# Kernel tuning notes

Measured on AMD Instinct MI355X. Metric: run time of the kernel, lower is better.

## Reference

```python
import jax, jax.numpy as jnp
import numpy as np

N = 100000   # nodes
E = 1000000  # edges (before self-loops)
G = 64       # graphs in batch
IN, HID, OUT = 128, 64, 1


def setup_inputs() -> dict:
    key = jax.random.key(0)
    ks = jax.random.split(key, 24)
    inp = {
        "x": jax.random.normal(ks[0], (N, IN), jnp.float32),
        "adj": jax.random.randint(ks[1], (2, E), 0, N, jnp.int32),
        "batch": jnp.sort(jax.random.randint(ks[2], (N,), 0, G, jnp.int32)),
    }
    i = 3
    dims = [(IN, HID), (HID, HID), (HID, HID)]
    for l, (di, do) in enumerate(dims, start=1):
        inp[f"W{l}"] = jax.random.normal(ks[i], (di, do), jnp.float32) * (1.0 / np.sqrt(di)); i += 1
        inp[f"a_src{l}"] = jax.random.normal(ks[i], (do,), jnp.float32) * 0.1; i += 1
        inp[f"a_dst{l}"] = jax.random.normal(ks[i], (do,), jnp.float32) * 0.1; i += 1
        inp[f"b{l}"] = jnp.zeros((do,), jnp.float32); i += 1
    inp["linnews_W"] = jax.random.normal(ks[i], (IN, HID), jnp.float32) * (1.0 / np.sqrt(IN)); i += 1
    inp["linnews_b"] = jnp.zeros((HID,), jnp.float32)
    inp["lin0_W"] = jax.random.normal(ks[i], (HID, HID), jnp.float32) * (1.0 / np.sqrt(HID)); i += 1
    inp["lin0_b"] = jnp.zeros((HID,), jnp.float32)
    inp["lin1_W"] = jax.random.normal(ks[i], (2 * HID, OUT), jnp.float32) * (1.0 / np.sqrt(2 * HID)); i += 1
    inp["lin1_b"] = jnp.zeros((OUT,), jnp.float32)
    return inp


def _gat_layer(x, src, dst, W, a_src, a_dst, b):
    # PyG GATConv, heads=1, self-loops already appended to (src, dst).
    h = x @ W                                        # [N, HID]
    e = (h @ a_src)[src] + (h @ a_dst)[dst]          # [E'] edge scores
    e = jax.nn.leaky_relu(e, 0.2)
    # segment softmax over incoming edges of each dst node
    m = jax.ops.segment_max(e, dst, num_segments=N)
    num = jnp.exp(e - m[dst])
    den = jax.ops.segment_sum(num, dst, num_segments=N)
    coef = num / (den[dst] + 1e-16)                  # [E']
    out = jax.ops.segment_sum(coef[:, None] * h[src], dst, num_segments=N)
    return out + b


def reference(x, adj, batch, W1, a_src1, a_dst1, b1, W2, a_src2, a_dst2, b2,
              W3, a_src3, a_dst3, b3, linnews_W, linnews_b, lin0_W, lin0_b,
              lin1_W, lin1_b):
    loop = jnp.arange(N, dtype=adj.dtype)
    src = jnp.concatenate([adj[0], loop])
    dst = jnp.concatenate([adj[1], loop])

    h = jax.nn.relu(_gat_layer(x, src, dst, W1, a_src1, a_dst1, b1))
    h = jax.nn.relu(_gat_layer(h, src, dst, W2, a_src2, a_dst2, b2))
    h = jax.nn.relu(_gat_layer(h, src, dst, W3, a_src3, a_dst3, b3))

    # global max pool per graph
    h = jax.ops.segment_max(h, batch, num_segments=G)        # [G, HID]
    h = jax.nn.relu(h @ lin0_W + lin0_b)

    # root node of each graph = first index with that batch id
    root = jax.ops.segment_min(jnp.arange(N), batch, num_segments=G)  # [G]
    news = jax.nn.relu(x[root] @ linnews_W + linnews_b)      # [G, HID]

    out = jnp.concatenate([h, news], axis=-1) @ lin1_W + lin1_b
    return jax.nn.sigmoid(out)                               # [G, 1]
```

## Files before the change

kernel.cpp:

```cpp
#include <hip/hip_runtime.h>
#include <hip/hip_fp16.h>
#include <cstdint>
#include <type_traits>

#define THREADS 256
#define NBLK 64
#define BPAD 512
#define LINBLK 640
#define ECAP 1024

typedef _Float16 half8 __attribute__((ext_vector_type(8)));
typedef float v4f __attribute__((ext_vector_type(4)));
typedef float v2f __attribute__((ext_vector_type(2)));

__global__ __launch_bounds__(256) void hist_kernel(const int* __restrict__ dst_e,
                                                   int* __restrict__ hist, int E, int chunk,
                                                   float* __restrict__ pool, int* __restrict__ root,
                                                   int G) {
  __shared__ int hcnt[BPAD];
  int t = threadIdx.x, blk = blockIdx.x;
  if (blk == 0) {
    for (int i = t; i < G * 64; i += 256) pool[i] = 0.0f;
    for (int i = t; i < G; i += 256) root[i] = 0x7fffffff;
  }
  for (int i = t; i < BPAD; i += 256) hcnt[i] = 0;
  __syncthreads();
  int s = blk * chunk, e = s + chunk;
  if (e > E) e = E;
  for (int i = s + t; i < e; i += 256) atomicAdd(&hcnt[dst_e[i] >> 8], 1);
  __syncthreads();
  for (int b = t; b < BPAD; b += 256) hist[b * NBLK + blk] = hcnt[b];
}

__global__ __launch_bounds__(256) void hscan_kernel(int* __restrict__ hist) {
  __shared__ int part[256];
  const int PER = (BPAD * NBLK) / 256;
  int t = threadIdx.x;
  int base = t * PER;
  int sum = 0;
  for (int k = 0; k < PER; k++) sum += hist[base + k];
  part[t] = sum;
  __syncthreads();
  int own = sum;
  for (int off = 1; off < 256; off <<= 1) {
    int v = (t >= off) ? part[t - off] : 0;
    __syncthreads();
    part[t] += v;
    __syncthreads();
  }
  int run = part[t] - own;
  for (int k = 0; k < PER; k++) {
    int h = hist[base + k];
    hist[base + k] = run;
    run += h;
  }
}

__global__ __launch_bounds__(256) void scatter_kernel(const int* __restrict__ src_e,
                                                      const int* __restrict__ dst_e,
                                                      const int* __restrict__ hist,
                                                      unsigned int* __restrict__ ebuf,
                                                      int E, int chunk) {
  __shared__ int cur[BPAD];
  int t = threadIdx.x, blk = blockIdx.x;
  for (int b = t; b < BPAD; b += 256) cur[b] = hist[b * NBLK + blk];
  __syncthreads();
  int s = blk * chunk, e = s + chunk;
  if (e > E) e = E;
  for (int i = s + t; i < e; i += 256) {
    int d = dst_e[i];
    unsigned int sv = (unsigned int)src_e[i];
    int slot = atomicAdd(&cur[d >> 8], 1);
    ebuf[slot] = (sv << 8) | (unsigned int)(d & 255);
  }
}

__global__ __launch_bounds__(256) void build_kernel(const unsigned int* __restrict__ ebuf,
                                                    const int* __restrict__ hist,
                                                    int* __restrict__ row_start,
                                                    int* __restrict__ csr_src,
                                                    int N, int E) {
  __shared__ int counts[256];
  __shared__ int sc[256];
  __shared__ int curw[256];
  int t = threadIdx.x, b = blockIdx.x;
  int nbase = b * 256;
  int ebase = hist[b * NBLK];
  int eend = hist[(b + 1) * NBLK];
  counts[t] = 0;
  __syncthreads();
  int ecount = eend - ebase;
  for (int i = t; i < ecount; i += 256)
    atomicAdd(&counts[ebuf[ebase + i] & 255u], 1);
  __syncthreads();
  int n = nbase + t;
  int val = (n < N) ? counts[t] + 1 : 0;
  sc[t] = val;
  __syncthreads();
  int own = val;
  for (int off = 1; off < 256; off <<= 1) {
    int v = (t >= off) ? sc[t - off] : 0;
    __syncthreads();
    sc[t] += v;
    __syncthreads();
  }
  int myloc = sc[t] - own;
  int rowb = ebase + nbase;
  if (n < N) {
    row_start[n] = rowb + myloc;
    csr_src[rowb + myloc + counts[t]] = n;
    if (n == N - 1) row_start[N] = rowb + myloc + counts[t] + 1;
  }
  curw[t] = rowb + myloc;
  __syncthreads();
  for (int i = t; i < ecount; i += 256) {
    unsigned int ev = ebuf[ebase + i];
    int pos = atomicAdd(&curw[ev & 255u], 1);
    csr_src[pos] = (int)(ev >> 8);
  }
}

__device__ __forceinline__ void store_row_fp8(const _Float16* hp, unsigned char* dst) {
  unsigned int d[4];
#pragma unroll
  for (int q = 0; q < 4; q++) {
    float f0 = (float)hp[q * 4 + 0], f1 = (float)hp[q * 4 + 1];
    float f2 = (float)hp[q * 4 + 2], f3 = (float)hp[q * 4 + 3];
    unsigned int w0 = __builtin_amdgcn_cvt_pk_fp8_f32(f0, f1, 0, false);
    d[q] = __builtin_amdgcn_cvt_pk_fp8_f32(f2, f3, w0, true);
  }
  uint4 v; v.x = d[0]; v.y = d[1]; v.z = d[2]; v.w = d[3];
  *(uint4*)dst = v;
}

template <int K, typename TIN>
__global__ __launch_bounds__(256) void lin_attn_kernel(
    const TIN* __restrict__ in, const float* __restrict__ W,
    const float* __restrict__ a_src, const float* __restrict__ a_dst,
    unsigned char* __restrict__ h8, float* __restrict__ as_, float* __restrict__ ad_,
    int N, int nwaves) {
  constexpr int NKC = K / 32;
  __shared__ _Float16 sh[4][16 * 72];
  const int t = threadIdx.x;
  const int lane = t & 63, w = t >> 6;
  const int col = lane & 15, quad = lane >> 4;
  const int wid = blockIdx.x * 4 + w;

  half8 bf[4][NKC];
#pragma unroll
  for (int nt = 0; nt < 4; nt++)
#pragma unroll
    for (int kc = 0; kc < NKC; kc++) {
      half8 v;
#pragma unroll
      for (int j = 0; j < 8; j++)
        v[j] = (_Float16)W[(kc * 32 + quad * 8 + j) * 64 + nt * 16 + col];
      bf[nt][kc] = v;
    }
  float sa[4], sd[4];
#pragma unroll
  for (int nt = 0; nt < 4; nt++) {
    sa[nt] = a_src[nt * 16 + col];
    sd[nt] = a_dst[nt * 16 + col];
  }

  const int ntiles = (N + 15) >> 4;
  for (int tile = wid; tile < ntiles; tile += nwaves) {
    const int nb = tile << 4;
    int nodeA = nb + col;
    if (nodeA >= N) nodeA = N - 1;
    const TIN* arow = in + (size_t)nodeA * K + quad * 8;

    v4f acc[4];
#pragma unroll
    for (int nt = 0; nt < 4; nt++) acc[nt] = (v4f){0.f, 0.f, 0.f, 0.f};

#pragma unroll
    for (int kc = 0; kc < NKC; kc++) {
      half8 a;
      if constexpr (std::is_same<TIN, float>::value) {
        float4 f0 = *(const float4*)(arow + kc * 32);
        float4 f1 = *(const float4*)(arow + kc * 32 + 4);
        a[0] = (_Float16)f0.x; a[1] = (_Float16)f0.y;
        a[2] = (_Float16)f0.z; a[3] = (_Float16)f0.w;
        a[4] = (_Float16)f1.x; a[5] = (_Float16)f1.y;
        a[6] = (_Float16)f1.z; a[7] = (_Float16)f1.w;
      } else {
        a = *(const half8*)(arow + kc * 32);
      }
#pragma unroll
      for (int nt = 0; nt < 4; nt++)
        acc[nt] = __builtin_amdgcn_mfma_f32_16x16x32_f16(a, bf[nt][kc], acc[nt], 0, 0, 0);
    }

    float ps[4], pd[4];
#pragma unroll
    for (int r = 0; r < 4; r++) { ps[r] = 0.f; pd[r] = 0.f; }
#pragma unroll
    for (int nt = 0; nt < 4; nt++)
#pragma unroll
      for (int r = 0; r < 4; r++) {
        ps[r] += acc[nt][r] * sa[nt];
        pd[r] += acc[nt][r] * sd[nt];
      }
#pragma unroll
    for (int r = 0; r < 4; r++)
#pragma unroll
      for (int m = 1; m < 16; m <<= 1) {
        ps[r] += __shfl_xor(ps[r], m);
        pd[r] += __shfl_xor(pd[r], m);
      }
    if (col == 0) {
#pragma unroll
      for (int r = 0; r < 4; r++) {
        int node = nb + quad * 4 + r;
        if (node < N) { as_[node] = ps[r]; ad_[node] = pd[r]; }
      }
    }

#pragma unroll
    for (int nt = 0; nt < 4; nt++)
#pragma unroll
      for (int r = 0; r < 4; r++)
        sh[w][(quad * 4 + r) * 72 + nt * 16 + col] = (_Float16)acc[nt][r];
    int nr = lane >> 2, c4 = lane & 3;
    int node = nb + nr;
    if (node < N)
      store_row_fp8(&sh[w][nr * 72 + c4 * 16], h8 + (size_t)node * 64 + c4 * 16);
  }
}

__device__ __forceinline__ void agg_block_stage(
    const uint2* __restrict__ h8v, const float* __restrict__ as_in,
    const int* __restrict__ csr_src, int* __restrict__ s_src,
    float* __restrict__ s_as, int t, int co,
    int e0, int eEnd, int rs, int re, float adn,
    float4& A0, float4& A1, float& den) {
  bool first = true;
  for (int cs = e0; cs < eEnd; cs += ECAP) {
    int ce = cs + ECAP; if (ce > eEnd) ce = eEnd;
    int cnt = ce - cs;
    if (!first) __syncthreads();
    first = false;
    for (int i = t; i < cnt; i += 512) {
      int s0 = csr_src[cs + i];
      bool has2 = (i + 256 < cnt);
      int s1 = has2 ? csr_src[cs + i + 256] : s0;
      float av0 = as_in[s0];
      float av1 = as_in[s1];
      s_src[i] = s0; s_as[i] = av0;
      if (has2) { s_src[i + 256] = s1; s_as[i + 256] = av1; }
    }
    __syncthreads();
    int a0 = rs > cs ? rs : cs;
    int a1 = re < ce ? re : ce;
    if (a0 >= a1) continue;

    auto loadhv = [&](int sb, uint2* hv) {
#pragma unroll
      for (int j = 0; j < 4; j++) {
        int sj = sb + j;
        int ii = ((sj < a1) ? sj : (a1 - 1)) - cs;
        hv[j] = h8v[(size_t)s_src[ii] * 8 + co];
      }
    };
    auto consume = [&](int sb, const uint2* hv) {
#pragma unroll
      for (int j = 0; j < 4; j++) {
        int sj = sb + j;
        int ii = ((sj < a1) ? sj : (a1 - 1)) - cs;
        float e = s_as[ii] + adn;
        e = fmaxf(e, 0.2f * e);
        float c = (sj < a1) ? __expf(e) : 0.f;
        v2f f0 = __builtin_amdgcn_cvt_pk_f32_fp8(hv[j].x, false);
        v2f f1 = __builtin_amdgcn_cvt_pk_f32_fp8(hv[j].x, true);
        v2f f2 = __builtin_amdgcn_cvt_pk_f32_fp8(hv[j].y, false);
        v2f f3 = __builtin_amdgcn_cvt_pk_f32_fp8(hv[j].y, true);
        den += c;
        A0.x += c * f0[0]; A0.y += c * f0[1]; A0.z += c * f1[0]; A0.w += c * f1[1];
        A1.x += c * f2[0]; A1.y += c * f2[1]; A1.z += c * f3[0]; A1.w += c * f3[1];
      }
    };

    uint2 hvA[4];
    int s = a0;
    loadhv(s, hvA);
    for (s = a0 + 4; s < a1; s += 4) {
      uint2 hvB[4];
      loadhv(s, hvB);
      consume(s - 4, hvA);
#pragma unroll
      for (int j = 0; j < 4; j++) hvA[j] = hvB[j];
    }
    consume(s - 4, hvA);
  }
}

__device__ __forceinline__ void agg_finish(const float4& A0, const float4& A1,
                                           float den, const float* __restrict__ bprev,
                                           int co, _Float16* o) {
  float inv = 1.0f / (den + 1e-16f);
  float4 b0 = *(const float4*)&bprev[co * 8];
  float4 b1 = *(const float4*)&bprev[co * 8 + 4];
  o[0] = (_Float16)fmaxf(A0.x * inv + b0.x, 0.f);
  o[1] = (_Float16)fmaxf(A0.y * inv + b0.y, 0.f);
  o[2] = (_Float16)fmaxf(A0.z * inv + b0.z, 0.f);
  o[3] = (_Float16)fmaxf(A0.w * inv + b0.w, 0.f);
  o[4] = (_Float16)fmaxf(A1.x * inv + b1.x, 0.f);
  o[5] = (_Float16)fmaxf(A1.y * inv + b1.y, 0.f);
  o[6] = (_Float16)fmaxf(A1.z * inv + b1.z, 0.f);
  o[7] = (_Float16)fmaxf(A1.w * inv + b1.w, 0.f);
}

__global__ __launch_bounds__(256) void agg_lin_kernel(
    const uint2* __restrict__ h8in, const float* __restrict__ as_in,
    const float* __restrict__ ad_in, const int* __restrict__ csr_src,
    const int* __restrict__ row_start, const float* __restrict__ bprev,
    const float* __restrict__ W, const float* __restrict__ a_src,
    const float* __restrict__ a_dst, unsigned char* __restrict__ h8out,
    float* __restrict__ as_out, float* __restrict__ ad_out, int N) {
  __shared__ int s_src[ECAP];
  __shared__ float s_as[ECAP];
  __shared__ _Float16 shh[32][72];
  __shared__ _Float16 sht[2][16 * 72];
  const int t = threadIdx.x;
  const int lane = t & 63, w = t >> 6;
  const int base = blockIdx.x * 32;

  {
    const int ng = lane >> 3, co = lane & 7;
    const int ln = w * 8 + ng;
    int n = base + ln;
    int nc = (n < N) ? n : (N - 1);
    int rs = row_start[nc], re = row_start[nc + 1];
    float adn = ad_in[nc];
    int nend = base + 32; if (nend > N) nend = N;
    int e0 = row_start[base], eEnd = row_start[nend];
    float4 A0 = make_float4(0.f, 0.f, 0.f, 0.f);
    float4 A1 = make_float4(0.f, 0.f, 0.f, 0.f);
    float den = 0.f;
    agg_block_stage(h8in, as_in, csr_src, s_src, s_as, t, co,
                    e0, eEnd, rs, re, adn, A0, A1, den);
    _Float16 o[8];
    agg_finish(A0, A1, den, bprev, co, o);
    *(float4*)&shh[ln][co * 8] = *(float4*)o;
  }
  __syncthreads();
  if (w >= 2) return;

  const int col = lane & 15, quad = lane >> 4;
  half8 bf[4][2];
  float sa[4], sd[4];
#pragma unroll
  for (int nt = 0; nt < 4; nt++) {
#pragma unroll
    for (int kc = 0; kc < 2; kc++) {
      half8 v;
#pragma unroll
      for (int j = 0; j < 8; j++)
        v[j] = (_Float16)W[(kc * 32 + quad * 8 + j) * 64 + nt * 16 + col];
      bf[nt][kc] = v;
    }
    sa[nt] = a_src[nt * 16 + col];
    sd[nt] = a_dst[nt * 16 + col];
  }

  const int nb = base + w * 16;
  v4f acc[4];
#pragma unroll
  for (int nt = 0; nt < 4; nt++) acc[nt] = (v4f){0.f, 0.f, 0.f, 0.f};
#pragma unroll
  for (int kc = 0; kc < 2; kc++) {
    half8 a = *(const half8*)&shh[w * 16 + col][kc * 32 + quad * 8];
#pragma unroll
    for (int nt = 0; nt < 4; nt++)
      acc[nt] = __builtin_amdgcn_mfma_f32_16x16x32_f16(a, bf[nt][kc], acc[nt], 0, 0, 0);
  }

  float ps[4], pd[4];
#pragma unroll
  for (int r = 0; r < 4; r++) { ps[r] = 0.f; pd[r] = 0.f; }
#pragma unroll
  for (int nt = 0; nt < 4; nt++)
#pragma unroll
    for (int r = 0; r < 4; r++) {
      ps[r] += acc[nt][r] * sa[nt];
      pd[r] += acc[nt][r] * sd[nt];
    }
#pragma unroll
  for (int r = 0; r < 4; r++)
#pragma unroll
    for (int m = 1; m < 16; m <<= 1) {
      ps[r] += __shfl_xor(ps[r], m);
      pd[r] += __shfl_xor(pd[r], m);
    }
  if (col == 0) {
#pragma unroll
    for (int r = 0; r < 4; r++) {
      int node = nb + quad * 4 + r;
      if (node < N) { as_out[node] = ps[r]; ad_out[node] = pd[r]; }
    }
  }

#pragma unroll
  for (int nt = 0; nt < 4; nt++)
#pragma unroll
    for (int r = 0; r < 4; r++)
      sht[w][(quad * 4 + r) * 72 + nt * 16 + col] = (_Float16)acc[nt][r];
  int nr = lane >> 2, c4 = lane & 3;
  int node = nb + nr;
  if (node < N)
    store_row_fp8(&sht[w][nr * 72 + c4 * 16], h8out + (size_t)node * 64 + c4 * 16);
}

__global__ __launch_bounds__(256) void agg_pool_kernel(
    const uint2* __restrict__ h8in, const float* __restrict__ as_in,
    const float* __restrict__ ad_in, const int* __restrict__ csr_src,
    const int* __restrict__ row_start, const float* __restrict__ bprev,
    const int* __restrict__ batch, float* __restrict__ pool,
    int* __restrict__ root, int N) {
  __shared__ int s_src[ECAP];
  __shared__ float s_as[ECAP];
  __shared__ float red[4][64];
  const int t = threadIdx.x;
  const int lane = t & 63, w = t >> 6;
  const int ng = lane >> 3, co = lane & 7;
  const int ln = w * 8 + ng;
  const int base = blockIdx.x * 32;
  int n = base + ln;
  int nc = (n < N) ? n : (N - 1);
  int rs = row_start[nc], re = row_start[nc + 1];
  float adn = ad_in[nc];
  int nend = base + 32; if (nend > N) nend = N;
  int e0 = row_start[base], eEnd = row_start[nend];
  float4 A0 = make_float4(0.f, 0.f, 0.f, 0.f);
  float4 A1 = make_float4(0.f, 0.f, 0.f, 0.f);
  float den = 0.f;
  agg_block_stage(h8in, as_in, csr_src, s_src, s_as, t, co,
                  e0, eEnd, rs, re, adn, A0, A1, den);
  _Float16 o[8];
  agg_finish(A0, A1, den, bprev, co, o);
  float ov[8];
#pragma unroll
  for (int j = 0; j < 8; j++) ov[j] = (float)o[j];

  int g = batch[nc];
  if (co == 0 && n < N) {
    if (n == 0 || batch[n - 1] != g) atomicMin(&root[g], n);
  }

  int bstart = base;
  int bend = base + 31; if (bend >= N) bend = N - 1;
  int gfirst = batch[bstart];
  int glast = batch[bend];
  if (gfirst == glast) {
#pragma unroll
    for (int m = 8; m < 64; m <<= 1)
#pragma unroll
      for (int j = 0; j < 8; j++) ov[j] = fmaxf(ov[j], __shfl_xor(ov[j], m));
    if (ng == 0)
#pragma unroll
      for (int j = 0; j < 8; j++) red[w][co * 8 + j] = ov[j];
    __syncthreads();
    if (t < 64) {
      float m0 = fmaxf(red[0][t], red[1][t]);
      float m1 = fmaxf(red[2][t], red[3][t]);
      atomicMax((int*)&pool[(size_t)gfirst * 64 + t], __float_as_int(fmaxf(m0, m1)));
    }
  } else {
#pragma unroll
    for (int j = 0; j < 8; j++)
      if (n < N) atomicMax((int*)&pool[(size_t)g * 64 + co * 8 + j], __float_as_int(ov[j]));
  }
}

__global__ void final_kernel(const float* __restrict__ pool, const int* __restrict__ root,
                             const float* __restrict__ x,
                             const float* __restrict__ lin0_W, const float* __restrict__ lin0_b,
                             const float* __restrict__ linnews_W, const float* __restrict__ linnews_b,
                             const float* __restrict__ lin1_W, const float* __restrict__ lin1_b,
                             float* __restrict__ out, int G, int N) {
  int t = threadIdx.x;
  int lane = t & 63, w = t >> 6;
  int g = blockIdx.x * 4 + w;
  if (g >= G) return;
  float hp = 0.f;
  for (int k = 0; k < 64; k++) hp += pool[(size_t)g * 64 + k] * lin0_W[k * 64 + lane];
  hp = fmaxf(hp + lin0_b[lane], 0.f);
  int r = root[g]; if (r > N - 1) r = N - 1; if (r < 0) r = 0;
  float nw = 0.f;
  for (int k = 0; k < 128; k++) nw += x[(size_t)r * 128 + k] * linnews_W[k * 64 + lane];
  nw = fmaxf(nw + linnews_b[lane], 0.f);
  float p = hp * lin1_W[lane] + nw * lin1_W[64 + lane];
  for (int k = 1; k < 64; k <<= 1) p += __shfl_xor(p, k);
  if (lane == 0) out[g] = 1.0f / (1.0f + __expf(-(p + lin1_b[0])));
}

extern "C" void kernel_launch(void* const* d_in, const int* in_sizes, int n_in,
                              void* d_out, int out_size, void* d_ws, size_t ws_size,
                              hipStream_t stream) {
  (void)n_in; (void)ws_size;
  const float* x      = (const float*)d_in[0];
  const int*   adj    = (const int*)d_in[1];
  const int*   batch  = (const int*)d_in[2];
  const float* W1     = (const float*)d_in[3];
  const float* asrc1  = (const float*)d_in[4];
  const float* adst1  = (const float*)d_in[5];
  const float* b1     = (const float*)d_in[6];
  const float* W2     = (const float*)d_in[7];
  const float* asrc2  = (const float*)d_in[8];
  const float* adst2  = (const float*)d_in[9];
  const float* b2     = (const float*)d_in[10];
  const float* W3     = (const float*)d_in[11];
  const float* asrc3  = (const float*)d_in[12];
  const float* adst3  = (const float*)d_in[13];
  const float* b3     = (const float*)d_in[14];
  const float* lnW    = (const float*)d_in[15];
  const float* lnb    = (const float*)d_in[16];
  const float* l0W    = (const float*)d_in[17];
  const float* l0b    = (const float*)d_in[18];
  const float* l1W    = (const float*)d_in[19];
  const float* l1b    = (const float*)d_in[20];
  float* outp = (float*)d_out;

  const int N = in_sizes[2];
  const int E = in_sizes[1] / 2;
  const int Etot = E + N;
  const int G = out_size;
  const int B = (N + 255) / 256;

  const int* src_e = adj;
  const int* dst_e = adj + E;

  uintptr_t p = (uintptr_t)d_ws;
  auto alloc = [&](size_t bytes) -> void* {
    void* r = (void*)p;
    p += (bytes + 255) & ~(size_t)255;
    return r;
  };
  int*      hist      = (int*)alloc((size_t)BPAD * NBLK * 4);
  int*      row_start = (int*)alloc((size_t)(N + 1) * 4);
  int*      csr_src   = (int*)alloc((size_t)Etot * 4);
  unsigned int* ebuf  = (unsigned int*)alloc((size_t)E * 4);
  unsigned char* hA   = (unsigned char*)alloc((size_t)N * 64);
  unsigned char* hB   = (unsigned char*)alloc((size_t)N * 64);
  float*    asA       = (float*)alloc((size_t)N * 4);
  float*    adA       = (float*)alloc((size_t)N * 4);
  float*    asB       = (float*)alloc((size_t)N * 4);
  float*    adB       = (float*)alloc((size_t)N * 4);
  float*    pool      = (float*)alloc((size_t)G * 64 * 4);
  int*      root      = (int*)alloc((size_t)G * 4);

  int chunk = (E + NBLK - 1) / NBLK;
  hist_kernel<<<dim3(NBLK), dim3(256), 0, stream>>>(dst_e, hist, E, chunk, pool, root, G);
  hscan_kernel<<<dim3(1), dim3(256), 0, stream>>>(hist);
  scatter_kernel<<<dim3(NBLK), dim3(256), 0, stream>>>(src_e, dst_e, hist, ebuf, E, chunk);
  build_kernel<<<dim3(B), dim3(256), 0, stream>>>(ebuf, hist, row_start, csr_src, N, E);

  const int aggGrid = (N + 31) / 32;
  const int nwaves = LINBLK * 4;

  lin_attn_kernel<128, float><<<dim3(LINBLK), dim3(256), 0, stream>>>(
      x, W1, asrc1, adst1, hA, asA, adA, N, nwaves);
  agg_lin_kernel<<<dim3(aggGrid), dim3(256), 0, stream>>>(
      (const uint2*)hA, asA, adA, csr_src, row_start, b1, W2, asrc2, adst2, hB, asB, adB, N);
  agg_lin_kernel<<<dim3(aggGrid), dim3(256), 0, stream>>>(
      (const uint2*)hB, asB, adB, csr_src, row_start, b2, W3, asrc3, adst3, hA, asA, adA, N);
  agg_pool_kernel<<<dim3(aggGrid), dim3(256), 0, stream>>>(
      (const uint2*)hA, asA, adA, csr_src, row_start, b3, batch, pool, root, N);

  final_kernel<<<dim3((G + 3) / 4), dim3(256), 0, stream>>>(
      pool, root, x, l0W, l0b, lnW, lnb, l1W, l1b, outp, G, N);
}
```

Measured before the change: 294.7 us.

## Split layer-1 linear projection across CSR-build kernels as extra blocks

Removes the standalone layer-1 linear/attention kernel and splits its node tiles into four quarters. Each quarter runs on extra blocks appended to one of the four CSR-construction kernels (hist, scan, scatter, build). The aim is to fill the mostly idle GPU during those low-occupancy graph-building kernels and drop one launch. The cost is more shared memory and registers in those kernels, and the build work may now compete with the matmul blocks for compute units.

```diff
diff --git a/kernel.cpp b/kernel.cpp
--- a/kernel.cpp
+++ b/kernel.cpp
@@ -6,19 +6,129 @@
 #define THREADS 256
 #define NBLK 64
 #define BPAD 512
-#define LINBLK 640
 #define ECAP 1024
+#define LINB 392
 
 typedef _Float16 half8 __attribute__((ext_vector_type(8)));
 typedef float v4f __attribute__((ext_vector_type(4)));
 typedef float v2f __attribute__((ext_vector_type(2)));
 
-__global__ __launch_bounds__(256) void hist_kernel(const int* __restrict__ dst_e,
-                                                   int* __restrict__ hist, int E, int chunk,
-                                                   float* __restrict__ pool, int* __restrict__ root,
-                                                   int G) {
+__device__ __forceinline__ void store_row_fp8(const _Float16* hp, unsigned char* dst) {
+  unsigned int d[4];
+#pragma unroll
+  for (int q = 0; q < 4; q++) {
+    float f0 = (float)hp[q * 4 + 0], f1 = (float)hp[q * 4 + 1];
+    float f2 = (float)hp[q * 4 + 2], f3 = (float)hp[q * 4 + 3];
+    unsigned int w0 = __builtin_amdgcn_cvt_pk_fp8_f32(f0, f1, 0, false);
+    d[q] = __builtin_amdgcn_cvt_pk_fp8_f32(f2, f3, w0, true);
+  }
+  uint4 v; v.x = d[0]; v.y = d[1]; v.z = d[2]; v.w = d[3];
+  *(uint4*)dst = v;
+}
+
+__device__ __forceinline__ void lin1_run(
+    const float* __restrict__ in, const float* __restrict__ W,
+    const float* __restrict__ a_src, const float* __restrict__ a_dst,
+    unsigned char* __restrict__ h8, float* __restrict__ as_, float* __restrict__ ad_,
+    int N, int tile0, int tile1, int wid, int nwaves, _Float16* shw) {
+  const int lane = threadIdx.x & 63;
+  const int col = lane & 15, quad = lane >> 4;
+
+  half8 bf[4][4];
+#pragma unroll
+  for (int nt = 0; nt < 4; nt++)
+#pragma unroll
+    for (int kc = 0; kc < 4; kc++) {
+      half8 v;
+#pragma unroll
+      for (int j = 0; j < 8; j++)
+        v[j] = (_Float16)W[(kc * 32 + quad * 8 + j) * 64 + nt * 16 + col];
+      bf[nt][kc] = v;
+    }
+  float sa[4], sd[4];
+#pragma unroll
+  for (int nt = 0; nt < 4; nt++) {
+    sa[nt] = a_src[nt * 16 + col];
+    sd[nt] = a_dst[nt * 16 + col];
+  }
+
+  for (int tile = tile0 + wid; tile < tile1; tile += nwaves) {
+    const int nb = tile << 4;
+    int nodeA = nb + col;
+    if (nodeA >= N) nodeA = N - 1;
+    const float* arow = in + (size_t)nodeA * 128 + quad * 8;
+
+    v4f acc[4];
+#pragma unroll
+    for (int nt = 0; nt < 4; nt++) acc[nt] = (v4f){0.f, 0.f, 0.f, 0.f};
+
+#pragma unroll
+    for (int kc = 0; kc < 4; kc++) {
+      float4 f0 = *(const float4*)(arow + kc * 32);
+      float4 f1 = *(const float4*)(arow + kc * 32 + 4);
+      half8 a;
+      a[0] = (_Float16)f0.x; a[1] = (_Float16)f0.y;
+      a[2] = (_Float16)f0.z; a[3] = (_Float16)f0.w;
+      a[4] = (_Float16)f1.x; a[5] = (_Float16)f1.y;
+      a[6] = (_Float16)f1.z; a[7] = (_Float16)f1.w;
+#pragma unroll
+      for (int nt = 0; nt < 4; nt++)
+        acc[nt] = __builtin_amdgcn_mfma_f32_16x16x32_f16(a, bf[nt][kc], acc[nt], 0, 0, 0);
+    }
+
+    float ps[4], pd[4];
+#pragma unroll
+    for (int r = 0; r < 4; r++) { ps[r] = 0.f; pd[r] = 0.f; }
+#pragma unroll
+    for (int nt = 0; nt < 4; nt++)
+#pragma unroll
+      for (int r = 0; r < 4; r++) {
+        ps[r] += acc[nt][r] * sa[nt];
+        pd[r] += acc[nt][r] * sd[nt];
+      }
+#pragma unroll
+    for (int r = 0; r < 4; r++)
+#pragma unroll
+      for (int m = 1; m < 16; m <<= 1) {
+        ps[r] += __shfl_xor(ps[r], m);
+        pd[r] += __shfl_xor(pd[r], m);
+      }
+    if (col == 0) {
+#pragma unroll
+      for (int r = 0; r < 4; r++) {
+        int node = nb + quad * 4 + r;
+        if (node < N) { as_[node] = ps[r]; ad_[node] = pd[r]; }
+      }
+    }
+
+#pragma unroll
+    for (int nt = 0; nt < 4; nt++)
+#pragma unroll
+      for (int r = 0; r < 4; r++)
+        shw[(quad * 4 + r) * 72 + nt * 16 + col] = (_Float16)acc[nt][r];
+    int nr = lane >> 2, c4 = lane & 3;
+    int node = nb + nr;
+    if (node < N)
+      store_row_fp8(&shw[nr * 72 + c4 * 16], h8 + (size_t)node * 64 + c4 * 16);
+  }
+}
+
+#define LIN_ARGS const float* __restrict__ x, const float* __restrict__ W1, \
+                 const float* __restrict__ a1s, const float* __restrict__ a1d, \
+                 unsigned char* __restrict__ h8, float* __restrict__ lin_as, \
+                 float* __restrict__ lin_ad, int Nn, int tile0, int tile1, int nlw
+
+__global__ __launch_bounds__(256) void hist_lin_kernel(
+    const int* __restrict__ dst_e, int* __restrict__ hist, int E, int chunk,
+    float* __restrict__ pool, int* __restrict__ root, int G, LIN_ARGS) {
   __shared__ int hcnt[BPAD];
+  __shared__ _Float16 sh[4][16 * 72];
   int t = threadIdx.x, blk = blockIdx.x;
+  if (blk >= NBLK) {
+    int wid = (blk - NBLK) * 4 + (t >> 6);
+    lin1_run(x, W1, a1s, a1d, h8, lin_as, lin_ad, Nn, tile0, tile1, wid, nlw, sh[t >> 6]);
+    return;
+  }
   if (blk == 0) {
     for (int i = t; i < G * 64; i += 256) pool[i] = 0.0f;
     for (int i = t; i < G; i += 256) root[i] = 0x7fffffff;
@@ -32,10 +142,16 @@
   for (int b = t; b < BPAD; b += 256) hist[b * NBLK + blk] = hcnt[b];
 }
 
-__global__ __launch_bounds__(256) void hscan_kernel(int* __restrict__ hist) {
+__global__ __launch_bounds__(256) void hscan_lin_kernel(int* __restrict__ hist, LIN_ARGS) {
   __shared__ int part[256];
+  __shared__ _Float16 sh[4][16 * 72];
+  int t = threadIdx.x, blk = blockIdx.x;
+  if (blk >= 1) {
+    int wid = (blk - 1) * 4 + (t >> 6);
+    lin1_run(x, W1, a1s, a1d, h8, lin_as, lin_ad, Nn, tile0, tile1, wid, nlw, sh[t >> 6]);
+    return;
+  }
   const int PER = (BPAD * NBLK) / 256;
-  int t = threadIdx.x;
   int base = t * PER;
   int sum = 0;
   for (int k = 0; k < PER; k++) sum += hist[base + k];
@@ -56,13 +172,18 @@
   }
 }
 
-__global__ __launch_bounds__(256) void scatter_kernel(const int* __restrict__ src_e,
-                                                      const int* __restrict__ dst_e,
-                                                      const int* __restrict__ hist,
-                                                      unsigned int* __restrict__ ebuf,
-                                                      int E, int chunk) {
+__global__ __launch_bounds__(256) void scatter_lin_kernel(
+    const int* __restrict__ src_e, const int* __restrict__ dst_e,
+    const int* __restrict__ hist, unsigned int* __restrict__ ebuf,
+    int E, int chunk, LIN_ARGS) {
   __shared__ int cur[BPAD];
+  __shared__ _Float16 sh[4][16 * 72];
   int t = threadIdx.x, blk = blockIdx.x;
+  if (blk >= NBLK) {
+    int wid = (blk - NBLK) * 4 + (t >> 6);
+    lin1_run(x, W1, a1s, a1d, h8, lin_as, lin_ad, Nn, tile0, tile1, wid, nlw, sh[t >> 6]);
+    return;
+  }
   for (int b = t; b < BPAD; b += 256) cur[b] = hist[b * NBLK + blk];
   __syncthreads();
   int s = blk * chunk, e = s + chunk;
@@ -75,15 +196,20 @@
   }
 }
 
-__global__ __launch_bounds__(256) void build_kernel(const unsigned int* __restrict__ ebuf,
-                                                    const int* __restrict__ hist,
-                                                    int* __restrict__ row_start,
-                                                    int* __restrict__ csr_src,
-                                                    int N, int E) {
+__global__ __launch_bounds__(256) void build_lin_kernel(
+    const unsigned int* __restrict__ ebuf, const int* __restrict__ hist,
+    int* __restrict__ row_start, int* __restrict__ csr_src,
+    int N, int E, int BB, LIN_ARGS) {
   __shared__ int counts[256];
   __shared__ int sc[256];
   __shared__ int curw[256];
+  __shared__ _Float16 sh[4][16 * 72];
   int t = threadIdx.x, b = blockIdx.x;
+  if (b >= BB) {
+    int wid = (b - BB) * 4 + (t >> 6);
+    lin1_run(x, W1, a1s, a1d, h8, lin_as, lin_ad, Nn, tile0, tile1, wid, nlw, sh[t >> 6]);
+    return;
+  }
   int nbase = b * 256;
   int ebase = hist[b * NBLK];
   int eend = hist[(b + 1) * NBLK];
@@ -117,116 +243,6 @@
     unsigned int ev = ebuf[ebase + i];
     int pos = atomicAdd(&curw[ev & 255u], 1);
     csr_src[pos] = (int)(ev >> 8);
-  }
-}
-
-__device__ __forceinline__ void store_row_fp8(const _Float16* hp, unsigned char* dst) {
-  unsigned int d[4];
-#pragma unroll
-  for (int q = 0; q < 4; q++) {
-    float f0 = (float)hp[q * 4 + 0], f1 = (float)hp[q * 4 + 1];
-    float f2 = (float)hp[q * 4 + 2], f3 = (float)hp[q * 4 + 3];
-    unsigned int w0 = __builtin_amdgcn_cvt_pk_fp8_f32(f0, f1, 0, false);
-    d[q] = __builtin_amdgcn_cvt_pk_fp8_f32(f2, f3, w0, true);
-  }
-  uint4 v; v.x = d[0]; v.y = d[1]; v.z = d[2]; v.w = d[3];
-  *(uint4*)dst = v;
-}
-
-template <int K, typename TIN>
-__global__ __launch_bounds__(256) void lin_attn_kernel(
-    const TIN* __restrict__ in, const float* __restrict__ W,
-    const float* __restrict__ a_src, const float* __restrict__ a_dst,
-    unsigned char* __restrict__ h8, float* __restrict__ as_, float* __restrict__ ad_,
-    int N, int nwaves) {
-  constexpr int NKC = K / 32;
-  __shared__ _Float16 sh[4][16 * 72];
-  const int t = threadIdx.x;
-  const int lane = t & 63, w = t >> 6;
-  const int col = lane & 15, quad = lane >> 4;
-  const int wid = blockIdx.x * 4 + w;
-
-  half8 bf[4][NKC];
-#pragma unroll
-  for (int nt = 0; nt < 4; nt++)
-#pragma unroll
-    for (int kc = 0; kc < NKC; kc++) {
-      half8 v;
-#pragma unroll
-      for (int j = 0; j < 8; j++)
-        v[j] = (_Float16)W[(kc * 32 + quad * 8 + j) * 64 + nt * 16 + col];
-      bf[nt][kc] = v;
-    }
-  float sa[4], sd[4];
-#pragma unroll
-  for (int nt = 0; nt < 4; nt++) {
-    sa[nt] = a_src[nt * 16 + col];
-    sd[nt] = a_dst[nt * 16 + col];
-  }
-
-  const int ntiles = (N + 15) >> 4;
-  for (int tile = wid; tile < ntiles; tile += nwaves) {
-    const int nb = tile << 4;
-    int nodeA = nb + col;
-    if (nodeA >= N) nodeA = N - 1;
-    const TIN* arow = in + (size_t)nodeA * K + quad * 8;
-
-    v4f acc[4];
-#pragma unroll
-    for (int nt = 0; nt < 4; nt++) acc[nt] = (v4f){0.f, 0.f, 0.f, 0.f};
-
-#pragma unroll
-    for (int kc = 0; kc < NKC; kc++) {
-      half8 a;
-      if constexpr (std::is_same<TIN, float>::value) {
-        float4 f0 = *(const float4*)(arow + kc * 32);
-        float4 f1 = *(const float4*)(arow + kc * 32 + 4);
-        a[0] = (_Float16)f0.x; a[1] = (_Float16)f0.y;
-        a[2] = (_Float16)f0.z; a[3] = (_Float16)f0.w;
-        a[4] = (_Float16)f1.x; a[5] = (_Float16)f1.y;
-        a[6] = (_Float16)f1.z; a[7] = (_Float16)f1.w;
-      } else {
-        a = *(const half8*)(arow + kc * 32);
-      }
-#pragma unroll
-      for (int nt = 0; nt < 4; nt++)
-        acc[nt] = __builtin_amdgcn_mfma_f32_16x16x32_f16(a, bf[nt][kc], acc[nt], 0, 0, 0);
-    }
-
-    float ps[4], pd[4];
-#pragma unroll
-    for (int r = 0; r < 4; r++) { ps[r] = 0.f; pd[r] = 0.f; }
-#pragma unroll
-    for (int nt = 0; nt < 4; nt++)
-#pragma unroll
-      for (int r = 0; r < 4; r++) {
-        ps[r] += acc[nt][r] * sa[nt];
-        pd[r] += acc[nt][r] * sd[nt];
-      }
-#pragma unroll
-    for (int r = 0; r < 4; r++)
-#pragma unroll
-      for (int m = 1; m < 16; m <<= 1) {
-        ps[r] += __shfl_xor(ps[r], m);
-        pd[r] += __shfl_xor(pd[r], m);
-      }
-    if (col == 0) {
-#pragma unroll
-      for (int r = 0; r < 4; r++) {
-        int node = nb + quad * 4 + r;
-        if (node < N) { as_[node] = ps[r]; ad_[node] = pd[r]; }
-      }
-    }
-
-#pragma unroll
-    for (int nt = 0; nt < 4; nt++)
-#pragma unroll
-      for (int r = 0; r < 4; r++)
-        sh[w][(quad * 4 + r) * 72 + nt * 16 + col] = (_Float16)acc[nt][r];
-    int nr = lane >> 2, c4 = lane & 3;
-    int node = nb + nr;
-    if (node < N)
-      store_row_fp8(&sh[w][nr * 72 + c4 * 16], h8 + (size_t)node * 64 + c4 * 16);
   }
 }
 
@@ -552,16 +568,24 @@
   int*      root      = (int*)alloc((size_t)G * 4);
 
   int chunk = (E + NBLK - 1) / NBLK;
-  hist_kernel<<<dim3(NBLK), dim3(256), 0, stream>>>(dst_e, hist, E, chunk, pool, root, G);
-  hscan_kernel<<<dim3(1), dim3(256), 0, stream>>>(hist);
-  scatter_kernel<<<dim3(NBLK), dim3(256), 0, stream>>>(src_e, dst_e, hist, ebuf, E, chunk);
-  build_kernel<<<dim3(B), dim3(256), 0, stream>>>(ebuf, hist, row_start, csr_src, N, E);
+  const int ntiles = (N + 15) >> 4;
+  const int nlw = LINB * 4;
+  const int c1 = ntiles / 4, c2 = ntiles / 2, c3 = (3 * ntiles) / 4;
+
+  hist_lin_kernel<<<dim3(NBLK + LINB), dim3(256), 0, stream>>>(
+      dst_e, hist, E, chunk, pool, root, G,
+      x, W1, asrc1, adst1, hA, asA, adA, N, 0, c1, nlw);
+  hscan_lin_kernel<<<dim3(1 + LINB), dim3(256), 0, stream>>>(
+      hist, x, W1, asrc1, adst1, hA, asA, adA, N, c1, c2, nlw);
+  scatter_lin_kernel<<<dim3(NBLK + LINB), dim3(256), 0, stream>>>(
+      src_e, dst_e, hist, ebuf, E, chunk,
+      x, W1, asrc1, adst1, hA, asA, adA, N, c2, c3, nlw);
+  build_lin_kernel<<<dim3(B + LINB), dim3(256), 0, stream>>>(
+      ebuf, hist, row_start, csr_src, N, E, B,
+      x, W1, asrc1, adst1, hA, asA, adA, N, c3, ntiles, nlw);
 
   const int aggGrid = (N + 31) / 32;
-  const int nwaves = LINBLK * 4;
-
-  lin_attn_kernel<128, float><<<dim3(LINBLK), dim3(256), 0, stream>>>(
-      x, W1, asrc1, adst1, hA, asA, adA, N, nwaves);
+
   agg_lin_kernel<<<dim3(aggGrid), dim3(256), 0, stream>>>(
       (const uint2*)hA, asA, adA, csr_src, row_start, b1, W2, asrc2, adst2, hB, asB, adB, N);
   agg_lin_kernel<<<dim3(aggGrid), dim3(256), 0, stream>>>(
```

Measured after the change: 290.2 us. No clear change (-1.5%).
